# Kernel tuning notes

Measured on AMD Instinct MI355X. Metric: run time of the kernel, lower is better.

The kernel has to match this reference:

```python
import jax, jax.numpy as jnp
import numpy as np

EPS = 1e-5

def _gconv(x, src, dst, w_rel, w_root, b):
    # PyG GraphConv (aggr='add'): out = lin_rel(sum_j x_j) + lin_root(x)
    agg = jax.ops.segment_sum(x[src], dst, num_segments=x.shape[0])
    return agg @ w_rel + x @ w_root + b

def _bn(x, g, b, m, v):
    # BatchNorm1d in eval mode (running stats)
    return g * (x - m) * jax.lax.rsqrt(v + EPS) + b

def setup_inputs() -> dict:
    key = jax.random.key(0)
    ks = jax.random.split(key, 32)
    N, E, F, H, G = 100000, 2000000, 32, 40, 512
    inp = {}
    inp['x'] = jax.random.normal(ks[0], (N, F), dtype=jnp.float32)
    inp['edge_index'] = jax.random.randint(ks[1], (2, E), 0, N, dtype=jnp.int64)
    inp['edge_attr'] = jax.random.uniform(ks[2], (E, 1), dtype=jnp.float32)
    inp['batch'] = jnp.sort(jax.random.randint(ks[3], (N,), 0, G, dtype=jnp.int64))
    inp['num_graphs'] = G
    s = 0.1
    inp['w1_rel'] = jax.random.normal(ks[4], (F, H), dtype=jnp.float32) * s
    inp['w1_root'] = jax.random.normal(ks[5], (F, H), dtype=jnp.float32) * s
    inp['b1'] = jnp.zeros((H,), dtype=jnp.float32)
    inp['w2_rel'] = jax.random.normal(ks[6], (H, H), dtype=jnp.float32) * s
    inp['w2_root'] = jax.random.normal(ks[7], (H, H), dtype=jnp.float32) * s
    inp['b2'] = jnp.zeros((H,), dtype=jnp.float32)
    inp['w3_rel'] = jax.random.normal(ks[8], (H, H), dtype=jnp.float32) * s
    inp['w3_root'] = jax.random.normal(ks[9], (H, H), dtype=jnp.float32) * s
    inp['b3'] = jnp.zeros((H,), dtype=jnp.float32)
    for i, k1, k2 in ((1, 10, 11), (2, 12, 13), (3, 14, 15)):
        inp[f'bn{i}_g'] = jnp.ones((H,), dtype=jnp.float32)
        inp[f'bn{i}_b'] = jnp.zeros((H,), dtype=jnp.float32)
        inp[f'bn{i}_m'] = jax.random.normal(ks[k1], (H,), dtype=jnp.float32) * 0.1
        inp[f'bn{i}_v'] = jax.random.uniform(ks[k2], (H,), dtype=jnp.float32) + 0.5
    inp['wl1'] = jax.random.normal(ks[16], (H, 10), dtype=jnp.float32) * s
    inp['bl1'] = jnp.zeros((10,), dtype=jnp.float32)
    inp['wl2'] = jax.random.normal(ks[17], (10, 1), dtype=jnp.float32) * s
    inp['bl2'] = jnp.zeros((1,), dtype=jnp.float32)
    return inp


def reference(x, edge_index, edge_attr, batch, num_graphs,
              w1_rel, w1_root, b1, bn1_g, bn1_b, bn1_m, bn1_v,
              w2_rel, w2_root, b2, bn2_g, bn2_b, bn2_m, bn2_v,
              w3_rel, w3_root, b3, bn3_g, bn3_b, bn3_m, bn3_v,
              wl1, bl1, wl2, bl2):
    src, dst = edge_index[0], edge_index[1]
    h = jax.nn.relu(_gconv(x, src, dst, w1_rel, w1_root, b1))
    h = _bn(h, bn1_g, bn1_b, bn1_m, bn1_v)
    h = jax.nn.relu(_gconv(h, src, dst, w2_rel, w2_root, b2))
    h = _bn(h, bn2_g, bn2_b, bn2_m, bn2_v)
    # dropout is identity in eval mode
    h = _gconv(h, src, dst, w3_rel, w3_root, b3)
    h = _bn(h, bn3_g, bn3_b, bn3_m, bn3_v)
    # global max pool over graphs
    gm = jax.ops.segment_max(h, batch, num_segments=num_graphs)
    gm = jnp.where(jnp.isfinite(gm), gm, 0.0)  # guard empty graphs
    out = jax.nn.relu(gm @ wl1 + bl1) @ wl2 + bl2
    return jax.nn.sigmoid(out)
```

## Files before the change

kernel.cpp:

```cpp
#include <hip/hip_runtime.h>
#include <math.h>

#define N_NODES  100000
#define N_EDGES  2000000
#define HID      40
#define N_GRAPHS 512

#define BK_SHIFT 6
#define BK_NODES 64
#define K_BUCK   ((N_NODES + BK_NODES - 1) / BK_NODES)
#define CAP8     384
#define NMAX     2048

typedef int v4i __attribute__((ext_vector_type(4)));


__global__ void k_bin8(const int* __restrict__ src, const int* __restrict__ dst,
                       int* __restrict__ cnt8, unsigned* __restrict__ bins8) {
    int e4 = blockIdx.x * blockDim.x + threadIdx.x;
    if (e4 >= N_EDGES / 4) return;
    v4i s4 = __builtin_nontemporal_load((const v4i*)src + e4);
    v4i d4 = __builtin_nontemporal_load((const v4i*)dst + e4);
    int sub = blockIdx.x & 7;
#pragma unroll
    for (int j = 0; j < 4; ++j) {
        int d = d4[j], s = s4[j];
        int b  = d >> BK_SHIFT;
        int dl = d & (BK_NODES - 1);
        int c  = sub * K_BUCK + b;
        int pos = atomicAdd(&cnt8[c], 1);
        if (pos < CAP8)
            bins8[(size_t)c * CAP8 + pos] = (unsigned)s | ((unsigned)dl << 17);
    }
}


__global__ __launch_bounds__(256)
void k_sortfill(const int* __restrict__ cnt8, const unsigned* __restrict__ bins8,
                int* __restrict__ csr, int* __restrict__ off, int* __restrict__ deg) {
    __shared__ unsigned els[NMAX];
    __shared__ int scnt[8], sbase[9];
    __shared__ int h[64], nb[64], cur[64];
    const int t = threadIdx.x, b = blockIdx.x;

    if (t < 8) { int c = cnt8[t * K_BUCK + b]; scnt[t] = (c > CAP8) ? CAP8 : c; }
    if (t < 64) { h[t] = 0; cur[t] = 0; }
    __syncthreads();
    if (t == 0) {
        int r = 0;
        for (int s = 0; s < 8; ++s) {
            sbase[s] = r;
            r += scnt[s];
            if (r > NMAX) r = NMAX;
        }
        sbase[8] = r;
    }
    __syncthreads();
    const int n = sbase[8];

    for (int s = 0; s < 8; ++s) {
        const unsigned* bp = bins8 + (size_t)(s * K_BUCK + b) * CAP8;
        int c = sbase[s + 1] - sbase[s];
        int base = sbase[s];
        for (int i = t; i < c; i += 256)
            els[base + i] = __builtin_nontemporal_load(bp + i);
    }
    __syncthreads();
    for (int i = t; i < n; i += 256) atomicAdd(&h[els[i] >> 17], 1);
    __syncthreads();
    if (t == 0) { int r = 0; for (int j = 0; j < 64; ++j) { nb[j] = r; r += h[j]; } }
    __syncthreads();
    const int cbase = b * NMAX;
    for (int i = t; i < n; i += 256) {
        unsigned p = els[i];
        int dl  = (int)(p >> 17);
        int pos = nb[dl] + atomicAdd(&cur[dl], 1);
        csr[cbase + pos] = (int)(p & 0x1FFFFu);
    }
    if (t < 64) {
        int node = (b << BK_SHIFT) + t;
        if (node < N_NODES) { off[node] = cbase + nb[t]; deg[node] = h[t]; }
    }
}


template<int F, bool RELU>
__global__ __launch_bounds__(320)
void k_agg_tf(const float* __restrict__ feat, const int* __restrict__ csr,
              const int* __restrict__ off, const int* __restrict__ deg,
              const float* __restrict__ w_rel, const float* __restrict__ w_root,
              const float* __restrict__ bias,
              const float* __restrict__ bn_g, const float* __restrict__ bn_b,
              const float* __restrict__ bn_m, const float* __restrict__ bn_v,
              float* __restrict__ h_out) {
    constexpr int R4  = F / 4;
    constexpr int NPB = 320 / R4;
    constexpr int KO  = HID / R4;
    constexpr int ST  = F + 4;

    __shared__ float accs[NPB][ST];
    __shared__ float xs[NPB][ST];
    __shared__ float wl[F * HID];
    __shared__ float wr[F * HID];
    __shared__ float bb[HID], sc[HID], sh[HID];

    const int t    = threadIdx.x;
    const int nl   = t / R4;
    const int f4   = t - nl * R4;
    const int node = blockIdx.x * NPB + nl;

    for (int i = t; i < F * HID; i += 320) { wl[i] = w_rel[i]; wr[i] = w_root[i]; }
    if (t < HID) {
        float s = bn_g[t] * rsqrtf(bn_v[t] + 1e-5f);
        sc[t] = s; sh[t] = bn_b[t] - bn_m[t] * s; bb[t] = bias[t];
    }

    const float4* feat4 = (const float4*)feat;
    float4 xv = feat4[(size_t)node * R4 + f4];
    *(float4*)&xs[nl][f4 * 4] = xv;

    const int s0 = off[node];
    const int e0 = s0 + deg[node];
    float4 acc = make_float4(0.f, 0.f, 0.f, 0.f);
    for (int k = s0; k < e0; k += 4) {
        int i0 = __builtin_nontemporal_load(csr + k);
        int i1 = __builtin_nontemporal_load(csr + ((k + 1 < e0) ? k + 1 : e0 - 1));
        int i2 = __builtin_nontemporal_load(csr + ((k + 2 < e0) ? k + 2 : e0 - 1));
        int i3 = __builtin_nontemporal_load(csr + ((k + 3 < e0) ? k + 3 : e0 - 1));
        float m1 = (k + 1 < e0) ? 1.f : 0.f;
        float m2 = (k + 2 < e0) ? 1.f : 0.f;
        float m3 = (k + 3 < e0) ? 1.f : 0.f;
        float4 v0 = feat4[(size_t)i0 * R4 + f4];
        float4 v1 = feat4[(size_t)i1 * R4 + f4];
        float4 v2 = feat4[(size_t)i2 * R4 + f4];
        float4 v3 = feat4[(size_t)i3 * R4 + f4];
        acc.x += v0.x;      acc.y += v0.y;      acc.z += v0.z;      acc.w += v0.w;
        acc.x += m1 * v1.x; acc.y += m1 * v1.y; acc.z += m1 * v1.z; acc.w += m1 * v1.w;
        acc.x += m2 * v2.x; acc.y += m2 * v2.y; acc.z += m2 * v2.z; acc.w += m2 * v2.w;
        acc.x += m3 * v3.x; acc.y += m3 * v3.y; acc.z += m3 * v3.z; acc.w += m3 * v3.w;
    }
    *(float4*)&accs[nl][f4 * 4] = acc;
    __syncthreads();

    float o[KO];
#pragma unroll
    for (int k2 = 0; k2 < KO; ++k2) o[k2] = bb[f4 * KO + k2];
    for (int i = 0; i < F; ++i) {
        float aa = accs[nl][i];
        float xa = xs[nl][i];
        const float* wli = &wl[i * HID + f4 * KO];
        const float* wri = &wr[i * HID + f4 * KO];
#pragma unroll
        for (int k2 = 0; k2 < KO; ++k2)
            o[k2] += aa * wli[k2] + xa * wri[k2];
    }
#pragma unroll
    for (int k2 = 0; k2 < KO; ++k2) {
        float v = o[k2];
        if (RELU) v = fmaxf(v, 0.f);
        o[k2] = sc[f4 * KO + k2] * v + sh[f4 * KO + k2];
    }
    float* op = h_out + (size_t)node * HID + f4 * KO;
#pragma unroll
    for (int k2 = 0; k2 < KO; ++k2) op[k2] = o[k2];
}


__global__ __launch_bounds__(256)
void k_pool_head(const float* __restrict__ h, const int* __restrict__ batch,
                 const float* __restrict__ wl1, const float* __restrict__ bl1,
                 const float* __restrict__ wl2, const float* __restrict__ bl2,
                 float* __restrict__ out) {
    int g = blockIdx.x;
    int lo = 0, hi = N_NODES;
    while (lo < hi) { int mid = (lo + hi) >> 1; if (batch[mid] < g) lo = mid + 1; else hi = mid; }
    int start = lo;
    hi = N_NODES;
    while (lo < hi) { int mid = (lo + hi) >> 1; if (batch[mid] < g + 1) lo = mid + 1; else hi = mid; }
    int end = lo;

    __shared__ float red[25][44];
    __shared__ float gm[HID];
    __shared__ float l1[10];
    int t = threadIdx.x;
    int grp = t / 10, j4 = t - grp * 10;
    if (t < 250) {
        float4 m4 = make_float4(-INFINITY, -INFINITY, -INFINITY, -INFINITY);
        for (int r = start + grp; r < end; r += 25) {
            float4 v = ((const float4*)(h + (size_t)r * HID))[j4];
            m4.x = fmaxf(m4.x, v.x); m4.y = fmaxf(m4.y, v.y);
            m4.z = fmaxf(m4.z, v.z); m4.w = fmaxf(m4.w, v.w);
        }
        *((float4*)&red[grp][j4 * 4]) = m4;
    }
    __syncthreads();
    if (t < HID) {
        float m = -INFINITY;
#pragma unroll
        for (int g2 = 0; g2 < 25; ++g2) m = fmaxf(m, red[g2][t]);
        gm[t] = isfinite(m) ? m : 0.f;
    }
    __syncthreads();
    if (t < 10) {
        float acc = bl1[t];
#pragma unroll
        for (int i = 0; i < HID; ++i) acc += gm[i] * wl1[i * 10 + t];
        l1[t] = fmaxf(acc, 0.f);
    }
    __syncthreads();
    if (t == 0) {
        float acc = bl2[0];
#pragma unroll
        for (int i = 0; i < 10; ++i) acc += l1[i] * wl2[i];
        out[g] = 1.f / (1.f + expf(-acc));
    }
}


extern "C" void kernel_launch(void* const* d_in, const int* in_sizes, int n_in,
                              void* d_out, int out_size, void* d_ws, size_t ws_size,
                              hipStream_t stream) {
    const float* x       = (const float*)d_in[0];
    const int*   ei      = (const int*)d_in[1];
    const int*   src     = ei;
    const int*   dst     = ei + N_EDGES;
    const int*   batch   = (const int*)d_in[3];
    const float* w1_rel  = (const float*)d_in[5];
    const float* w1_root = (const float*)d_in[6];
    const float* b1      = (const float*)d_in[7];
    const float* w2_rel  = (const float*)d_in[8];
    const float* w2_root = (const float*)d_in[9];
    const float* b2      = (const float*)d_in[10];
    const float* w3_rel  = (const float*)d_in[11];
    const float* w3_root = (const float*)d_in[12];
    const float* b3      = (const float*)d_in[13];
    const float* bn1_g = (const float*)d_in[14], *bn1_b = (const float*)d_in[15];
    const float* bn1_m = (const float*)d_in[16], *bn1_v = (const float*)d_in[17];
    const float* bn2_g = (const float*)d_in[18], *bn2_b = (const float*)d_in[19];
    const float* bn2_m = (const float*)d_in[20], *bn2_v = (const float*)d_in[21];
    const float* bn3_g = (const float*)d_in[22], *bn3_b = (const float*)d_in[23];
    const float* bn3_m = (const float*)d_in[24], *bn3_v = (const float*)d_in[25];
    const float* wl1 = (const float*)d_in[26], *bl1 = (const float*)d_in[27];
    const float* wl2 = (const float*)d_in[28], *bl2 = (const float*)d_in[29];
    float* out = (float*)d_out;

    char* ws = (char*)d_ws;
    size_t o = 0;
    auto take = [&](size_t bytes) -> void* {
        void* p = ws + o;
        o = (o + bytes + 255) & ~(size_t)255;
        return p;
    };
    int*      cnt8  = (int*)take((size_t)K_BUCK * 8 * sizeof(int));
    unsigned* bins8 = (unsigned*)take((size_t)K_BUCK * 8 * CAP8 * sizeof(unsigned));
    int*      csr   = (int*)take((size_t)K_BUCK * NMAX * sizeof(int));
    int*      off   = (int*)take((size_t)N_NODES * sizeof(int));
    int*      deg   = (int*)take((size_t)N_NODES * sizeof(int));
    float*    hA    = (float*)take((size_t)N_NODES * HID * sizeof(float));
    float*    hB    = (float*)take((size_t)N_NODES * HID * sizeof(float));

    hipMemsetAsync(cnt8, 0, (size_t)K_BUCK * 8 * sizeof(int), stream);
    k_bin8<<<(N_EDGES / 4 + 255) / 256, 256, 0, stream>>>(src, dst, cnt8, bins8);
    k_sortfill<<<K_BUCK, 256, 0, stream>>>(cnt8, bins8, csr, off, deg);

    k_agg_tf<32, true><<<N_NODES / 40, 320, 0, stream>>>(
        x, csr, off, deg, w1_rel, w1_root, b1, bn1_g, bn1_b, bn1_m, bn1_v, hA);
    k_agg_tf<40, true><<<N_NODES / 32, 320, 0, stream>>>(
        hA, csr, off, deg, w2_rel, w2_root, b2, bn2_g, bn2_b, bn2_m, bn2_v, hB);
    k_agg_tf<40, false><<<N_NODES / 32, 320, 0, stream>>>(
        hB, csr, off, deg, w3_rel, w3_root, b3, bn3_g, bn3_b, bn3_m, bn3_v, hA);

    k_pool_head<<<N_GRAPHS, 256, 0, stream>>>(hA, batch, wl1, bl1, wl2, bl2, out);
}
```

Baseline: 430.1 us.

## Pad CSR rows to 8, vectorize neighbor index loads, bin by XCC id

```diff
diff --git a/kernel.cpp b/kernel.cpp
--- a/kernel.cpp
+++ b/kernel.cpp
@@ -11,6 +11,7 @@
 #define K_BUCK   ((N_NODES + BK_NODES - 1) / BK_NODES)
 #define CAP8     384
 #define NMAX     2048
+#define NMAX_PAD 2560
 
 typedef int v4i __attribute__((ext_vector_type(4)));
 
@@ -19,9 +20,11 @@
                        int* __restrict__ cnt8, unsigned* __restrict__ bins8) {
     int e4 = blockIdx.x * blockDim.x + threadIdx.x;
     if (e4 >= N_EDGES / 4) return;
+    unsigned xcc;
+    asm volatile("s_getreg_b32 %0, hwreg(HW_REG_XCC_ID)" : "=s"(xcc));
+    int sub = (int)(xcc & 7u);
     v4i s4 = __builtin_nontemporal_load((const v4i*)src + e4);
     v4i d4 = __builtin_nontemporal_load((const v4i*)dst + e4);
-    int sub = blockIdx.x & 7;
 #pragma unroll
     for (int j = 0; j < 4; ++j) {
         int d = d4[j], s = s4[j];
@@ -68,9 +71,12 @@
     __syncthreads();
     for (int i = t; i < n; i += 256) atomicAdd(&h[els[i] >> 17], 1);
     __syncthreads();
-    if (t == 0) { int r = 0; for (int j = 0; j < 64; ++j) { nb[j] = r; r += h[j]; } }
-    __syncthreads();
-    const int cbase = b * NMAX;
+    if (t == 0) {
+        int r = 0;
+        for (int j = 0; j < 64; ++j) { nb[j] = r; r += (h[j] + 7) & ~7; }
+    }
+    __syncthreads();
+    const int cbase = b * NMAX_PAD;
     for (int i = t; i < n; i += 256) {
         unsigned p = els[i];
         int dl  = (int)(p >> 17);
@@ -78,6 +84,8 @@
         csr[cbase + pos] = (int)(p & 0x1FFFFu);
     }
     if (t < 64) {
+        int pe = nb[t] + ((h[t] + 7) & ~7);
+        for (int i = nb[t] + h[t]; i < pe; ++i) csr[cbase + i] = 0;
         int node = (b << BK_SHIFT) + t;
         if (node < N_NODES) { off[node] = cbase + nb[t]; deg[node] = h[t]; }
     }
@@ -122,22 +130,32 @@
     const int s0 = off[node];
     const int e0 = s0 + deg[node];
     float4 acc = make_float4(0.f, 0.f, 0.f, 0.f);
-    for (int k = s0; k < e0; k += 4) {
-        int i0 = __builtin_nontemporal_load(csr + k);
-        int i1 = __builtin_nontemporal_load(csr + ((k + 1 < e0) ? k + 1 : e0 - 1));
-        int i2 = __builtin_nontemporal_load(csr + ((k + 2 < e0) ? k + 2 : e0 - 1));
-        int i3 = __builtin_nontemporal_load(csr + ((k + 3 < e0) ? k + 3 : e0 - 1));
+    for (int k = s0; k < e0; k += 8) {
+        v4i ca = __builtin_nontemporal_load((const v4i*)(csr + k));
+        v4i cb = __builtin_nontemporal_load((const v4i*)(csr + k + 4));
+        float4 v0 = feat4[(size_t)ca[0] * R4 + f4];
+        float4 v1 = feat4[(size_t)ca[1] * R4 + f4];
+        float4 v2 = feat4[(size_t)ca[2] * R4 + f4];
+        float4 v3 = feat4[(size_t)ca[3] * R4 + f4];
+        float4 v4_ = feat4[(size_t)cb[0] * R4 + f4];
+        float4 v5 = feat4[(size_t)cb[1] * R4 + f4];
+        float4 v6 = feat4[(size_t)cb[2] * R4 + f4];
+        float4 v7 = feat4[(size_t)cb[3] * R4 + f4];
         float m1 = (k + 1 < e0) ? 1.f : 0.f;
         float m2 = (k + 2 < e0) ? 1.f : 0.f;
         float m3 = (k + 3 < e0) ? 1.f : 0.f;
-        float4 v0 = feat4[(size_t)i0 * R4 + f4];
-        float4 v1 = feat4[(size_t)i1 * R4 + f4];
-        float4 v2 = feat4[(size_t)i2 * R4 + f4];
-        float4 v3 = feat4[(size_t)i3 * R4 + f4];
-        acc.x += v0.x;      acc.y += v0.y;      acc.z += v0.z;      acc.w += v0.w;
-        acc.x += m1 * v1.x; acc.y += m1 * v1.y; acc.z += m1 * v1.z; acc.w += m1 * v1.w;
-        acc.x += m2 * v2.x; acc.y += m2 * v2.y; acc.z += m2 * v2.z; acc.w += m2 * v2.w;
-        acc.x += m3 * v3.x; acc.y += m3 * v3.y; acc.z += m3 * v3.z; acc.w += m3 * v3.w;
+        float m4 = (k + 4 < e0) ? 1.f : 0.f;
+        float m5 = (k + 5 < e0) ? 1.f : 0.f;
+        float m6 = (k + 6 < e0) ? 1.f : 0.f;
+        float m7 = (k + 7 < e0) ? 1.f : 0.f;
+        acc.x += v0.x;       acc.y += v0.y;       acc.z += v0.z;       acc.w += v0.w;
+        acc.x += m1 * v1.x;  acc.y += m1 * v1.y;  acc.z += m1 * v1.z;  acc.w += m1 * v1.w;
+        acc.x += m2 * v2.x;  acc.y += m2 * v2.y;  acc.z += m2 * v2.z;  acc.w += m2 * v2.w;
+        acc.x += m3 * v3.x;  acc.y += m3 * v3.y;  acc.z += m3 * v3.z;  acc.w += m3 * v3.w;
+        acc.x += m4 * v4_.x; acc.y += m4 * v4_.y; acc.z += m4 * v4_.z; acc.w += m4 * v4_.w;
+        acc.x += m5 * v5.x;  acc.y += m5 * v5.y;  acc.z += m5 * v5.z;  acc.w += m5 * v5.w;
+        acc.x += m6 * v6.x;  acc.y += m6 * v6.y;  acc.z += m6 * v6.z;  acc.w += m6 * v6.w;
+        acc.x += m7 * v7.x;  acc.y += m7 * v7.y;  acc.z += m7 * v7.z;  acc.w += m7 * v7.w;
     }
     *(float4*)&accs[nl][f4 * 4] = acc;
     __syncthreads();
@@ -253,7 +271,7 @@
     };
     int*      cnt8  = (int*)take((size_t)K_BUCK * 8 * sizeof(int));
     unsigned* bins8 = (unsigned*)take((size_t)K_BUCK * 8 * CAP8 * sizeof(unsigned));
-    int*      csr   = (int*)take((size_t)K_BUCK * NMAX * sizeof(int));
+    int*      csr   = (int*)take((size_t)K_BUCK * NMAX_PAD * sizeof(int));
     int*      off   = (int*)take((size_t)N_NODES * sizeof(int));
     int*      deg   = (int*)take((size_t)N_NODES * sizeof(int));
     float*    hA    = (float*)take((size_t)N_NODES * HID * sizeof(float));
```

Result: faster. 415.5 us (-3.4%).
